# Kernel optimization log

Measured on AMD Instinct MI355X. Metric: run time of the kernel, lower is better.

## Reference

```python
import jax, jax.numpy as jnp
import numpy as np

B = 8192          # num_agents
IN_LEN = 20       # obs_len
PRED_LEN = 30     # output_len
H = 128           # h_dim
E = 64            # embedding_dim
D = 2             # data_dim
F_IN = IN_LEN * D # 40, ln1/spatial_embedding input features
LN_EPS = 1e-5


def setup_inputs() -> dict:
    key = jax.random.key(0)
    ks = jax.random.split(key, 8)
    def rn(i, shape, scale):
        return (jax.random.normal(ks[i], shape, jnp.float32) * scale).astype(jnp.float32)
    return dict(
        traj_abs=rn(0, (IN_LEN, B, D), 1.0),
        traj_rel=rn(1, (IN_LEN, B, D), 1.0),
        h0=rn(2, (1, B, H), 0.1),
        c0=rn(3, (1, B, H), 0.1),
        ln1_w=jnp.ones((F_IN,), jnp.float32),
        ln1_b=jnp.zeros((F_IN,), jnp.float32),
        emb_W=rn(4, (E, F_IN), 0.1),
        emb_b=jnp.zeros((E,), jnp.float32),
        W_ih=rn(5, (4 * H, E), 0.05),
        W_hh=rn(6, (4 * H, H), 0.05),
        b_ih=jnp.zeros((4 * H,), jnp.float32),
        b_hh=jnp.zeros((4 * H,), jnp.float32),
        ln2_w=jnp.ones((H,), jnp.float32),
        ln2_b=jnp.zeros((H,), jnp.float32),
        pos_W=rn(7, (D, H), 0.1),
        pos_b=jnp.zeros((D,), jnp.float32),
    )


def _layernorm(x, w, b):
    m = jnp.mean(x, axis=-1, keepdims=True)
    v = jnp.var(x, axis=-1, keepdims=True)
    return (x - m) * jax.lax.rsqrt(v + LN_EPS) * w + b


def reference(traj_abs, traj_rel, h0, c0, ln1_w, ln1_b, emb_W, emb_b,
              W_ih, W_hh, b_ih, b_hh, ln2_w, ln2_b, pos_W, pos_b):
    b = traj_rel.shape[1]
    h, c = h0[0], c0[0]  # num_layers=1 -> squeeze layer dim

    def step(carry, _):
        h, c, rel = carry
        # ln1 + spatial embedding + leaky_relu on raw C-order reshape (b, 40)
        x = _layernorm(rel.reshape(b, -1), ln1_w, ln1_b)
        x = jax.nn.leaky_relu(x @ emb_W.T + emb_b, negative_slope=0.01)
        # single LSTM step, torch gate order i, f, g, o
        gates = x @ W_ih.T + b_ih + h @ W_hh.T + b_hh  # (b, 4H)
        i, f, g, o = jnp.split(gates, 4, axis=-1)
        c_new = jax.nn.sigmoid(f) * c + jax.nn.sigmoid(i) * jnp.tanh(g)
        h_new = jax.nn.sigmoid(o) * jnp.tanh(c_new)
        # ln2 + hidden2pos
        rel_pos = _layernorm(h_new, ln2_w, ln2_b) @ pos_W.T + pos_b  # (b, 2)
        # roll window and write new rel position into last slot
        rel_new = jnp.concatenate([rel[1:], rel_pos[None]], axis=0)
        return (h_new, c_new, rel_new), rel_pos

    _, preds = jax.lax.scan(step, (h, c, traj_rel), None, length=PRED_LEN)
    return preds  # (pred_len, b, 2)
```

## Files before the change

### kernel.cpp

```cpp
#include <hip/hip_runtime.h>
#include <hip/hip_bf16.h>
#include <stdint.h>

#define K1 1.4426950408889634f
#define K2 2.8853900817779268f

typedef float f4 __attribute__((ext_vector_type(4)));
typedef float f2 __attribute__((ext_vector_type(2)));
typedef short s8v __attribute__((ext_vector_type(8)));
typedef unsigned int u32;
typedef unsigned short u16;

#define WS_WCAT  0
#define WS_WG    196608
#define WS_TE    204800
#define WS_SE    205056
#define WS_PWLN  205312
#define WS_SPW   206336
#define WS_PBE   206344
#define WS_BC    206352
#define WS_FLAGS 208400

#define C_WIN 0
#define C_RDY 1
#define C_RED 2
#define C_SWP 3
#define C_STT 4
#define C_PRD 5
#define C_FLG 6

__device__ __forceinline__ u16 f2bf(float x) {
    u32 u = __builtin_bit_cast(u32, x);
    u32 r = (u + 0x7FFFu + ((u >> 16) & 1u)) >> 16;
    return (u16)r;
}
__device__ __forceinline__ float bf2f(u16 h) {
    u32 u = ((u32)h) << 16;
    return __builtin_bit_cast(float, u);
}

__device__ __forceinline__ void waitge(u32* c, u32 v) {
    while (__hip_atomic_load(c, __ATOMIC_ACQUIRE, __HIP_MEMORY_SCOPE_WORKGROUP) < v) {}
}
__device__ __forceinline__ void waitge_s(u32* c, u32 v) {
    if (__hip_atomic_load(c, __ATOMIC_ACQUIRE, __HIP_MEMORY_SCOPE_WORKGROUP) >= v) return;
    do {
        __builtin_amdgcn_s_sleep(1);
    } while (__hip_atomic_load(c, __ATOMIC_ACQUIRE, __HIP_MEMORY_SCOPE_WORKGROUP) < v);
}
__device__ __forceinline__ void arrive(u32* c) {
    if ((threadIdx.x & 63) == 0)
        __hip_atomic_fetch_add(c, 1u, __ATOMIC_RELEASE, __HIP_MEMORY_SCOPE_WORKGROUP);
}

__global__ void prep_kernel(const float* __restrict__ ln1w, const float* __restrict__ ln1b,
                            const float* __restrict__ embW, const float* __restrict__ embB,
                            const float* __restrict__ Wih, const float* __restrict__ Whh,
                            const float* __restrict__ bih, const float* __restrict__ bhh,
                            const float* __restrict__ ln2w, const float* __restrict__ ln2b,
                            const float* __restrict__ posW, const float* __restrict__ posB,
                            char* __restrict__ ws) {
    const int tid = threadIdx.x;
    const int bid = blockIdx.x;
    u16* wcat = (u16*)(ws + WS_WCAT);

    if (bid > 0) {
        int base = (bid - 1) * 3072;
#pragma unroll 4
        for (int i = 0; i < 12; ++i) {
            int idx = base + i * 256 + tid;
            int np = idx / 192, k = idx % 192;
            int w = np >> 7, r = np & 127, nt = r >> 4, c = r & 15;
            int g = nt >> 1, jt = nt & 1;
            int n0 = (g << 7) | (w << 5) | (jt << 4) | c;
            float v = (k < 64) ? Wih[n0 * 64 + k] : Whh[n0 * 128 + (k - 64)];
            wcat[idx] = f2bf(v);
        }
        return;
    }

    u16* wg   = (u16*)(ws + WS_WG);
    float* te = (float*)(ws + WS_TE);
    float* se = (float*)(ws + WS_SE);
    float* pwln = (float*)(ws + WS_PWLN);
    float* spw  = (float*)(ws + WS_SPW);
    float* pbe  = (float*)(ws + WS_PBE);
    float* bc   = (float*)(ws + WS_BC);
    int* flags  = (int*)(ws + WS_FLAGS);
    __shared__ float pp[2][4];

    for (int idx = tid; idx < 64 * 64; idx += 256) {
        int e = idx >> 6, k = idx & 63;
        float v = (k < 40) ? embW[e * 40 + k] * ln1w[k] : 0.0f;
        wg[idx] = f2bf(v);
    }
    if (tid < 64) {
        int e = tid;
        float t = embB[e], s = 0.f;
        for (int k = 0; k < 40; ++k) {
            t += embW[e * 40 + k] * ln1b[k];
            s += bf2f(f2bf(embW[e * 40 + k] * ln1w[k]));
        }
        te[e] = t; se[e] = s;
    }
    if (tid >= 64 && tid < 192) {
        int j = tid - 64;
        float a0 = posW[j] * ln2w[j],      a1 = posW[128 + j] * ln2w[j];
        float b0 = posW[j] * ln2b[j],      b1 = posW[128 + j] * ln2b[j];
        pwln[j] = a0; pwln[128 + j] = a1;
#pragma unroll
        for (int m = 1; m < 64; m <<= 1) {
            a0 += __shfl_xor(a0, m, 64); a1 += __shfl_xor(a1, m, 64);
            b0 += __shfl_xor(b0, m, 64); b1 += __shfl_xor(b1, m, 64);
        }
        if ((tid & 63) == 0) {
            int wv = (tid >> 6) - 1;
            pp[wv][0] = a0; pp[wv][1] = a1; pp[wv][2] = b0; pp[wv][3] = b1;
        }
    }
    for (int idx = tid; idx < 512; idx += 256) {
        int w = idx >> 7, r = idx & 127, nt = r >> 4, c = r & 15;
        int g = nt >> 1, jt = nt & 1;
        int n0 = (g << 7) | (w << 5) | (jt << 4) | c;
        bc[idx] = bih[n0] + bhh[n0];
    }
    flags[tid] = 0;
    __syncthreads();
    if (tid == 0) {
        spw[0] = pp[0][0] + pp[1][0];
        spw[1] = pp[0][1] + pp[1][1];
        pbe[0] = posB[0] + pp[0][2] + pp[1][2];
        pbe[1] = posB[1] + pp[0][3] + pp[1][3];
    }
}

__global__ __launch_bounds__(512, 1)
void lstm_kernel(const float* __restrict__ traj_rel,
                 const float* __restrict__ h0, const float* __restrict__ c0,
                 float* __restrict__ dout, char* __restrict__ ws) {
    __shared__ __align__(16) u16 s_whh[12 * 512 * 8];
    __shared__ __align__(16) u16 s_x[2 * 8 * 32 * 8];
    __shared__ __align__(16) u16 s_h[2 * 16 * 32 * 8];
    __shared__ __align__(16) u16 s_win[2 * 8 * 32 * 8];
    __shared__ __align__(16) u16 s_pwb[2048];
    __shared__ __align__(16) float s_red1[4][4][32];
    __shared__ __align__(16) float s_red2[4][32];
    __shared__ __align__(16) f2 s_wp[320];
    __shared__ float s_mr[2][32][2];
    __shared__ float s_self[2][64];
    __shared__ u32 s_sync[8];

    const int tid = threadIdx.x;
    const int bk = blockIdx.x;
    const int lane = tid & 63;

    const u16* wcat = (const u16*)(ws + WS_WCAT);
    const u16* wg = (const u16*)(ws + WS_WG);
    int* flags = (int*)(ws + WS_FLAGS);

    if (tid == 0) {
        s_sync[C_WIN] = 0; s_sync[C_RDY] = 0; s_sync[C_RED] = 0;
        s_sync[C_SWP] = 0; s_sync[C_STT] = 0; s_sync[C_PRD] = 0;
        s_sync[C_FLG] = 0;
    }
    for (int idx = tid; idx < 12 * 512; idx += 512) {
        const u16* src = wcat + (idx & 511) * 192 + 96 + (idx >> 9) * 8;
        *(s8v*)(s_whh + idx * 8) = *(const s8v*)src;
    }
    {
        const float* pwln = (const float*)(ws + WS_PWLN);
        for (int idx = tid; idx < 2048; idx += 512) {
            int w = idx >> 9, rem = idx & 511;
            int ksub = rem >> 7, rem2 = rem & 127;
            int n = rem2 >> 3, i = rem2 & 7;
            int j = 32 * w + ksub * 8 + i;
            float v = (n == 0) ? 1.0f : (n == 1) ? pwln[j] : (n == 2) ? pwln[128 + j] : 0.0f;
            s_pwb[(((w * 4 + ksub) * 16) + n) * 8 + i] = f2bf(v);
        }
    }
    if (tid < 192) {
        int pb = tid / 96, r = tid % 96;
        int ch = 5 + r / 32, a = r & 31;
        s8v z = {0, 0, 0, 0, 0, 0, 0, 0};
        *(s8v*)(s_win + ((pb * 8 + ch) * 32 + a) * 8) = z;
    }
    if (tid < 320) {
        int p = 1280 * bk + 4 * tid;
        f4 v = *(const f4*)(traj_rel + p);
        int a = tid / 10, kq = (tid % 10) * 4;
        u32 lo = (u32)f2bf(v[0]) | ((u32)f2bf(v[1]) << 16);
        u32 hh = (u32)f2bf(v[2]) | ((u32)f2bf(v[3]) << 16);
        u32* dst = (u32*)(s_win + ((kq >> 3) * 32 + a) * 8 + (kq & 7));
        dst[0] = lo; dst[1] = hh;
        s_wp[tid] = f2{v[0] + v[1] + v[2] + v[3],
                       v[0] * v[0] + v[1] * v[1] + v[2] * v[2] + v[3] * v[3]};
    }
    if (tid < 256) {
        int a = tid & 31, q = tid >> 5;
        const float* hp = h0 + (bk * 32 + a) * 128 + q * 16;
        u16 hb[16];
#pragma unroll
        for (int u = 0; u < 16; ++u) hb[u] = f2bf(hp[u]);
#pragma unroll
        for (int half = 0; half < 2; ++half) {
            s8v v;
#pragma unroll
            for (int u = 0; u < 8; ++u) v[u] = (short)hb[half * 8 + u];
            *(s8v*)(s_h + ((2 * q + half) * 32 + a) * 8) = v;
        }
    }
    __syncthreads();
    if (tid < 32) {
        float s = 0.f, s2 = 0.f;
#pragma unroll
        for (int u = 0; u < 10; ++u) {
            f2 p = s_wp[tid * 10 + u];
            s += p[0]; s2 += p[1];
        }
        float m = s * (1.0f / 40.0f);
        float var = s2 * (1.0f / 40.0f) - m * m;
        s_mr[0][tid][0] = m;
        s_mr[0][tid][1] = __builtin_amdgcn_rsqf(var + 1e-5f);
    }
    __syncthreads();

    if (tid < 256) {
        const int wvi = tid >> 6;
        const int cx = lane & 15;
        const int hi4 = (lane >> 4) * 4;

        s8v wih[8][2], whhr[8];
#pragma unroll
        for (int nt = 0; nt < 8; ++nt) {
            int rowp = 128 * wvi + 16 * nt + cx;
#pragma unroll
            for (int kc = 0; kc < 2; ++kc)
                wih[nt][kc] = *(const s8v*)(wcat + rowp * 192 + kc * 32 + (lane >> 4) * 8);
            whhr[nt] = *(const s8v*)(wcat + rowp * 192 + 64 + (lane >> 4) * 8);
        }
        s8v wgf[2];
#pragma unroll
        for (int kc = 0; kc < 2; ++kc)
            wgf[kc] = *(const s8v*)(wg + (16 * wvi + cx) * 64 + kc * 32 + (lane >> 4) * 8);

        float se_l = ((const float*)(ws + WS_SE))[16 * wvi + cx];
        float te_l = ((const float*)(ws + WS_TE))[16 * wvi + cx];
        float bias[8];
#pragma unroll
        for (int nt = 0; nt < 8; ++nt)
            bias[nt] = ((const float*)(ws + WS_BC))[128 * wvi + 16 * nt + cx];
        float spw0 = ((const float*)(ws + WS_SPW))[0];
        float spw1 = ((const float*)(ws + WS_SPW))[1];
        float pbe0 = ((const float*)(ws + WS_PBE))[0];
        float pbe1 = ((const float*)(ws + WS_PBE))[1];

        float creg[2][2][4];
#pragma unroll
        for (int mt = 0; mt < 2; ++mt)
#pragma unroll
            for (int jt = 0; jt < 2; ++jt)
#pragma unroll
                for (int rg = 0; rg < 4; ++rg)
                    creg[mt][jt][rg] = c0[(bk * 32 + 16 * mt + hi4 + rg) * 128 + 32 * wvi + 16 * jt + cx];

        {
            f4 accE[2];
            accE[0] = f4{0.f, 0.f, 0.f, 0.f};
            accE[1] = f4{0.f, 0.f, 0.f, 0.f};
#pragma unroll
            for (int kc = 0; kc < 2; ++kc)
#pragma unroll
                for (int mt = 0; mt < 2; ++mt) {
                    s8v a = *(const s8v*)(s_win + ((kc * 4 + (lane >> 4)) * 32 + 16 * mt + cx) * 8);
                    accE[mt] = __builtin_amdgcn_mfma_f32_16x16x32_bf16(a, wgf[kc], accE[mt], 0, 0, 0);
                }
            int e = 16 * wvi + cx;
#pragma unroll
            for (int mt = 0; mt < 2; ++mt)
#pragma unroll
                for (int rg = 0; rg < 4; ++rg) {
                    int a = 16 * mt + hi4 + rg;
                    float m = s_mr[0][a][0], r = s_mr[0][a][1];
                    float x = r * (accE[mt][rg] - m * se_l) + te_l;
                    x = fmaxf(x, 0.f) + 0.01f * fminf(x, 0.f);
                    s_x[((e >> 3) * 32 + a) * 8 + (e & 7)] = f2bf(x);
                }
            arrive(&s_sync[C_RDY]);
        }

#pragma unroll 1
        for (int t = 0; t < 30; ++t) {
            const int pc = t & 1, pn = pc ^ 1;
            waitge(&s_sync[C_RDY], (u32)(4 * (t + 1)));

#pragma unroll
            for (int jt = 0; jt < 2; ++jt) {
                f4 acc[2][4];
#pragma unroll
                for (int mt = 0; mt < 2; ++mt)
#pragma unroll
                    for (int g = 0; g < 4; ++g) {
                        float b = bias[2 * g + jt];
                        acc[mt][g] = f4{b, b, b, b};
                    }
#pragma unroll
                for (int kc = 0; kc < 6; ++kc) {
                    s8v a0, a1;
                    if (kc < 2) {
                        a0 = *(const s8v*)(s_x + ((pc * 8 + kc * 4 + (lane >> 4)) * 32 + cx) * 8);
                        a1 = *(const s8v*)(s_x + ((pc * 8 + kc * 4 + (lane >> 4)) * 32 + 16 + cx) * 8);
                    } else {
                        int ch = (kc - 2) * 4 + (lane >> 4);
                        a0 = *(const s8v*)(s_h + ((pc * 16 + ch) * 32 + cx) * 8);
                        a1 = *(const s8v*)(s_h + ((pc * 16 + ch) * 32 + 16 + cx) * 8);
                    }
#pragma unroll
                    for (int g = 0; g < 4; ++g) {
                        int nt = 2 * g + jt;
                        s8v b;
                        if (kc < 2) b = wih[nt][kc];
                        else if (kc == 2) b = whhr[nt];
                        else b = *(const s8v*)(s_whh + (((kc - 3) * 4 + (lane >> 4)) * 512 + 128 * wvi + 16 * nt + cx) * 8);
                        acc[0][g] = __builtin_amdgcn_mfma_f32_16x16x32_bf16(a0, b, acc[0][g], 0, 0, 0);
                        acc[1][g] = __builtin_amdgcn_mfma_f32_16x16x32_bf16(a1, b, acc[1][g], 0, 0, 0);
                    }
                }
                int kk = 32 * wvi + 16 * jt + cx;
                int ch = pn * 16 + (kk >> 3);
#pragma unroll
                for (int mt = 0; mt < 2; ++mt)
#pragma unroll
                    for (int rg = 0; rg < 4; ++rg) {
                        float iv = acc[mt][0][rg];
                        float fv = acc[mt][1][rg];
                        float gv = acc[mt][2][rg];
                        float ov = acc[mt][3][rg];
                        float si = __builtin_amdgcn_rcpf(1.f + __builtin_amdgcn_exp2f(-K1 * iv));
                        float sf = __builtin_amdgcn_rcpf(1.f + __builtin_amdgcn_exp2f(-K1 * fv));
                        float so = __builtin_amdgcn_rcpf(1.f + __builtin_amdgcn_exp2f(-K1 * ov));
                        float tg = 1.f - 2.f * __builtin_amdgcn_rcpf(1.f + __builtin_amdgcn_exp2f(K2 * gv));
                        float cn = sf * creg[mt][jt][rg] + si * tg;
                        creg[mt][jt][rg] = cn;
                        float tc = 1.f - 2.f * __builtin_amdgcn_rcpf(1.f + __builtin_amdgcn_exp2f(K2 * cn));
                        float hn = so * tc;
                        int a = 16 * mt + hi4 + rg;
                        s_h[(ch * 32 + a) * 8 + (cx & 7)] = f2bf(hn);
                    }
            }

            {
                f4 d1[2], d2[2];
                d1[0] = f4{0.f, 0.f, 0.f, 0.f}; d1[1] = f4{0.f, 0.f, 0.f, 0.f};
                d2[0] = f4{0.f, 0.f, 0.f, 0.f}; d2[1] = f4{0.f, 0.f, 0.f, 0.f};
                s8v bfrag = *(const s8v*)(s_pwb + ((wvi * 4 + (lane >> 4)) * 16 + cx) * 8);
#pragma unroll
                for (int mt = 0; mt < 2; ++mt) {
                    s8v hf = *(const s8v*)(s_h + ((pn * 16 + 4 * wvi + (lane >> 4)) * 32 + 16 * mt + cx) * 8);
                    d1[mt] = __builtin_amdgcn_mfma_f32_16x16x32_bf16(hf, bfrag, d1[mt], 0, 0, 0);
                    d2[mt] = __builtin_amdgcn_mfma_f32_16x16x32_bf16(hf, hf, d2[mt], 0, 0, 0);
                }
#pragma unroll
                for (int mt = 0; mt < 2; ++mt) {
                    if (cx < 3) {
#pragma unroll
                        for (int rg = 0; rg < 4; ++rg)
                            s_red1[wvi][cx][mt * 16 + hi4 + rg] = d1[mt][rg];
                    }
                    if ((lane >> 4) == (cx >> 2))
                        s_red2[wvi][mt * 16 + cx] = d2[mt][cx & 3];
                }
            }
            arrive(&s_sync[C_RED]);

            if (wvi == 0) {
                waitge(&s_sync[C_RED], (u32)(4 * (t + 1)));
                int a = lane & 31, d = lane >> 5;
                float S0 = 0.f, S1 = 0.f, P = 0.f;
#pragma unroll
                for (int w = 0; w < 4; ++w) {
                    S0 += s_red1[w][0][a];
                    P  += s_red1[w][1 + d][a];
                    S1 += s_red2[w][a];
                }
                float m = S0 * (1.f / 128.f);
                float var = S1 * (1.f / 128.f) - m * m;
                float r = __builtin_amdgcn_rsqf(var + 1e-5f);
                float sp = (d == 0) ? spw0 : spw1;
                float pb = (d == 0) ? pbe0 : pbe1;
                float val = r * (P - m * sp) + pb;
                s_self[t & 1][2 * a + d] = val;
                if (tid == 0)
                    __hip_atomic_store(&s_sync[C_PRD], (u32)(t + 1), __ATOMIC_RELEASE, __HIP_MEMORY_SCOPE_WORKGROUP);
            }

            if (t < 29) {
                waitge(&s_sync[C_WIN], (u32)(t + 1));
                waitge(&s_sync[C_STT], (u32)(t + 1));
                f4 accE[2];
                accE[0] = f4{0.f, 0.f, 0.f, 0.f};
                accE[1] = f4{0.f, 0.f, 0.f, 0.f};
#pragma unroll
                for (int kc = 0; kc < 2; ++kc)
#pragma unroll
                    for (int mt = 0; mt < 2; ++mt) {
                        s8v a = *(const s8v*)(s_win + ((pn * 8 + kc * 4 + (lane >> 4)) * 32 + 16 * mt + cx) * 8);
                        accE[mt] = __builtin_amdgcn_mfma_f32_16x16x32_bf16(a, wgf[kc], accE[mt], 0, 0, 0);
                    }
                int e = 16 * wvi + cx;
#pragma unroll
                for (int mt = 0; mt < 2; ++mt)
#pragma unroll
                    for (int rg = 0; rg < 4; ++rg) {
                        int a = 16 * mt + hi4 + rg;
                        float m = s_mr[pn][a][0], r = s_mr[pn][a][1];
                        float x = r * (accE[mt][rg] - m * se_l) + te_l;
                        x = fmaxf(x, 0.f) + 0.01f * fminf(x, 0.f);
                        s_x[((pn * 8 + (e >> 3)) * 32 + a) * 8 + (e & 7)] = f2bf(x);
                    }
            }
            arrive(&s_sync[C_RDY]);
        }
    } else {
        const int gt = tid - 256;

        auto stage_one = [&](int ci, int s, int pb) {
            int p = 16384 * s + 1280 * bk + 4 * ci;
            float v0, v1, v2, v3;
            if (p < 327680) {
                f4 vv = *(const f4*)(traj_rel + p);
                v0 = vv[0]; v1 = vv[1]; v2 = vv[2]; v3 = vv[3];
            } else if (bk == 255 && ci >= 304) {
                waitge_s(&s_sync[C_PRD], (u32)s);
                int o = 4 * ci - 1216;
                const float* sf = &s_self[(s - 1) & 1][0];
                v0 = sf[o]; v1 = sf[o + 1]; v2 = sf[o + 2]; v3 = sf[o + 3];
            } else {
                waitge_s(&s_sync[C_FLG], (u32)s);
                int q = p - 327680;
                f4 vv = *(const f4*)(dout + q);
                v0 = vv[0]; v1 = vv[1]; v2 = vv[2]; v3 = vv[3];
            }
            int a = ci / 10, kq = (ci % 10) * 4;
            u32 lo = (u32)f2bf(v0) | ((u32)f2bf(v1) << 16);
            u32 hh = (u32)f2bf(v2) | ((u32)f2bf(v3) << 16);
            u32* dst = (u32*)(s_win + ((pb * 8 + (kq >> 3)) * 32 + a) * 8 + (kq & 7));
            dst[0] = lo; dst[1] = hh;
            s_wp[ci] = f2{v0 + v1 + v2 + v3, v0 * v0 + v1 * v1 + v2 * v2 + v3 * v3};
        };

#pragma unroll 1
        for (int u = 0; u < 29; ++u) {
            const int pb = (u + 1) & 1;
            waitge_s(&s_sync[C_STT], (u32)u);
            waitge_s(&s_sync[C_RDY], (u32)(4 * u));

            if (gt < 64) {
                int W0n = 16384 * (u + 1) + 1280 * bk;
                int Wend = W0n + 1280;
                if (Wend > 327680) {
                    int q0 = (W0n > 327680) ? (W0n - 327680) : 0;
                    int g = (q0 >> 6) + gt;
                    int gend = (Wend - 327681) >> 6;
                    if (g <= gend) {
                        int s = g >> 8, P = g & 255;
                        if (!(bk == 255 && P == 255)) {
                            while (__hip_atomic_load(&flags[P], __ATOMIC_RELAXED, __HIP_MEMORY_SCOPE_AGENT) <= s)
                                __builtin_amdgcn_s_sleep(2);
                        }
                    }
                }
                if (gt == 0)
                    __hip_atomic_store(&s_sync[C_FLG], (u32)(u + 1), __ATOMIC_RELEASE, __HIP_MEMORY_SCOPE_WORKGROUP);
            }

            stage_one(gt, u + 1, pb);
            if (gt < 64) stage_one(gt + 256, u + 1, pb);

            arrive(&s_sync[C_SWP]);

            if ((gt >> 6) == 1) {
                waitge_s(&s_sync[C_PRD], (u32)(u + 1));
                float val = s_self[u & 1][gt & 63];
                __hip_atomic_store(dout + u * 16384 + bk * 64 + (gt & 63), val,
                                   __ATOMIC_RELAXED, __HIP_MEMORY_SCOPE_AGENT);
                asm volatile("s_waitcnt vmcnt(0)" ::: "memory");
                if (gt == 64)
                    __hip_atomic_store(&flags[bk], u + 1, __ATOMIC_RELAXED, __HIP_MEMORY_SCOPE_AGENT);
            }

            if (gt < 64) {
                waitge_s(&s_sync[C_SWP], (u32)(4 * (u + 1)));
                if (gt == 0)
                    __hip_atomic_store(&s_sync[C_WIN], (u32)(u + 1), __ATOMIC_RELEASE, __HIP_MEMORY_SCOPE_WORKGROUP);
                if (gt < 32) {
                    float s = 0.f, s2 = 0.f;
#pragma unroll
                    for (int u2 = 0; u2 < 10; ++u2) {
                        f2 pp = s_wp[gt * 10 + u2];
                        s += pp[0]; s2 += pp[1];
                    }
                    float m = s * (1.0f / 40.0f);
                    float var = s2 * (1.0f / 40.0f) - m * m;
                    s_mr[pb][gt][0] = m;
                    s_mr[pb][gt][1] = __builtin_amdgcn_rsqf(var + 1e-5f);
                }
                if (gt == 0)
                    __hip_atomic_store(&s_sync[C_STT], (u32)(u + 1), __ATOMIC_RELEASE, __HIP_MEMORY_SCOPE_WORKGROUP);
            }
        }

        if ((gt >> 6) == 1) {
            waitge_s(&s_sync[C_PRD], 30u);
            float val = s_self[1][gt & 63];
            __hip_atomic_store(dout + 29 * 16384 + bk * 64 + (gt & 63), val,
                               __ATOMIC_RELAXED, __HIP_MEMORY_SCOPE_AGENT);
        }
    }
}

extern "C" void kernel_launch(void* const* d_in, const int* in_sizes, int n_in,
                              void* d_out, int out_size, void* d_ws, size_t ws_size,
                              hipStream_t stream) {
    (void)in_sizes; (void)n_in; (void)out_size; (void)ws_size;
    const float* traj_rel = (const float*)d_in[1];
    const float* h0 = (const float*)d_in[2];
    const float* c0 = (const float*)d_in[3];
    const float* ln1w = (const float*)d_in[4];
    const float* ln1b = (const float*)d_in[5];
    const float* embW = (const float*)d_in[6];
    const float* embB = (const float*)d_in[7];
    const float* Wih = (const float*)d_in[8];
    const float* Whh = (const float*)d_in[9];
    const float* bih = (const float*)d_in[10];
    const float* bhh = (const float*)d_in[11];
    const float* ln2w = (const float*)d_in[12];
    const float* ln2b = (const float*)d_in[13];
    const float* posW = (const float*)d_in[14];
    const float* posB = (const float*)d_in[15];
    char* ws = (char*)d_ws;

    hipLaunchKernelGGL(prep_kernel, dim3(33), dim3(256), 0, stream,
                       ln1w, ln1b, embW, embB, Wih, Whh, bih, bhh, ln2w, ln2b, posW, posB, ws);
    hipLaunchKernelGGL(lstm_kernel, dim3(256), dim3(512), 0, stream,
                       traj_rel, h0, c0, (float*)d_out, ws);
}
```

Measured before the change: 140.8 us.

## Split LSTM gate work across eight compute waves per block instead of four

Raises the block size from 512 to 768 threads so the recurrent gate MFMA work is spread over 8 waves, each handling one jt half of its wave-group's columns. Work after the gates is divided by jt: jt=0 waves do the LN2/projection reduction and jt=1 waves compute the next embedding. A new per-group barrier counter makes jt=0 wait for both halves' h writes. This aims to shorten the serial per-step critical path, at the cost of more synchronisation, more register pressure per SIMD and extra arrive counts.

```diff
diff --git a/kernel.cpp b/kernel.cpp
--- a/kernel.cpp
+++ b/kernel.cpp
@@ -28,6 +28,7 @@
 #define C_STT 4
 #define C_PRD 5
 #define C_FLG 6
+#define C_PW0 7
 
 __device__ __forceinline__ u16 f2bf(float x) {
     u32 u = __builtin_bit_cast(u32, x);
@@ -134,7 +135,7 @@
     }
 }
 
-__global__ __launch_bounds__(512, 1)
+__global__ __launch_bounds__(768, 1)
 void lstm_kernel(const float* __restrict__ traj_rel,
                  const float* __restrict__ h0, const float* __restrict__ c0,
                  float* __restrict__ dout, char* __restrict__ ws) {
@@ -148,7 +149,7 @@
     __shared__ __align__(16) f2 s_wp[320];
     __shared__ float s_mr[2][32][2];
     __shared__ float s_self[2][64];
-    __shared__ u32 s_sync[8];
+    __shared__ u32 s_sync[12];
 
     const int tid = threadIdx.x;
     const int bk = blockIdx.x;
@@ -158,18 +159,14 @@
     const u16* wg = (const u16*)(ws + WS_WG);
     int* flags = (int*)(ws + WS_FLAGS);
 
-    if (tid == 0) {
-        s_sync[C_WIN] = 0; s_sync[C_RDY] = 0; s_sync[C_RED] = 0;
-        s_sync[C_SWP] = 0; s_sync[C_STT] = 0; s_sync[C_PRD] = 0;
-        s_sync[C_FLG] = 0;
-    }
-    for (int idx = tid; idx < 12 * 512; idx += 512) {
+    if (tid < 12) s_sync[tid] = 0;
+    for (int idx = tid; idx < 12 * 512; idx += 768) {
         const u16* src = wcat + (idx & 511) * 192 + 96 + (idx >> 9) * 8;
         *(s8v*)(s_whh + idx * 8) = *(const s8v*)src;
     }
     {
         const float* pwln = (const float*)(ws + WS_PWLN);
-        for (int idx = tid; idx < 2048; idx += 512) {
+        for (int idx = tid; idx < 2048; idx += 768) {
             int w = idx >> 9, rem = idx & 511;
             int ksub = rem >> 7, rem2 = rem & 127;
             int n = rem2 >> 3, i = rem2 & 7;
@@ -224,19 +221,21 @@
     }
     __syncthreads();
 
-    if (tid < 256) {
-        const int wvi = tid >> 6;
+    if (tid < 512) {
+        const int w = tid >> 6;
+        const int wvi = w >> 1;
+        const int jt = w & 1;
         const int cx = lane & 15;
         const int hi4 = (lane >> 4) * 4;
 
-        s8v wih[8][2], whhr[8];
-#pragma unroll
-        for (int nt = 0; nt < 8; ++nt) {
-            int rowp = 128 * wvi + 16 * nt + cx;
+        s8v wih[4][2], whhr[4];
+#pragma unroll
+        for (int g = 0; g < 4; ++g) {
+            int rowp = 128 * wvi + 16 * (2 * g + jt) + cx;
 #pragma unroll
             for (int kc = 0; kc < 2; ++kc)
-                wih[nt][kc] = *(const s8v*)(wcat + rowp * 192 + kc * 32 + (lane >> 4) * 8);
-            whhr[nt] = *(const s8v*)(wcat + rowp * 192 + 64 + (lane >> 4) * 8);
+                wih[g][kc] = *(const s8v*)(wcat + rowp * 192 + kc * 32 + (lane >> 4) * 8);
+            whhr[g] = *(const s8v*)(wcat + rowp * 192 + 64 + (lane >> 4) * 8);
         }
         s8v wgf[2];
 #pragma unroll
@@ -245,25 +244,23 @@
 
         float se_l = ((const float*)(ws + WS_SE))[16 * wvi + cx];
         float te_l = ((const float*)(ws + WS_TE))[16 * wvi + cx];
-        float bias[8];
-#pragma unroll
-        for (int nt = 0; nt < 8; ++nt)
-            bias[nt] = ((const float*)(ws + WS_BC))[128 * wvi + 16 * nt + cx];
+        float bias[4];
+#pragma unroll
+        for (int g = 0; g < 4; ++g)
+            bias[g] = ((const float*)(ws + WS_BC))[128 * wvi + 16 * (2 * g + jt) + cx];
         float spw0 = ((const float*)(ws + WS_SPW))[0];
         float spw1 = ((const float*)(ws + WS_SPW))[1];
         float pbe0 = ((const float*)(ws + WS_PBE))[0];
         float pbe1 = ((const float*)(ws + WS_PBE))[1];
 
-        float creg[2][2][4];
+        float creg[2][4];
 #pragma unroll
         for (int mt = 0; mt < 2; ++mt)
 #pragma unroll
-            for (int jt = 0; jt < 2; ++jt)
-#pragma unroll
-                for (int rg = 0; rg < 4; ++rg)
-                    creg[mt][jt][rg] = c0[(bk * 32 + 16 * mt + hi4 + rg) * 128 + 32 * wvi + 16 * jt + cx];
-
-        {
+            for (int rg = 0; rg < 4; ++rg)
+                creg[mt][rg] = c0[(bk * 32 + 16 * mt + hi4 + rg) * 128 + 32 * wvi + 16 * jt + cx];
+
+        if (jt == 1) {
             f4 accE[2];
             accE[0] = f4{0.f, 0.f, 0.f, 0.f};
             accE[1] = f4{0.f, 0.f, 0.f, 0.f};
@@ -285,46 +282,43 @@
                     x = fmaxf(x, 0.f) + 0.01f * fminf(x, 0.f);
                     s_x[((e >> 3) * 32 + a) * 8 + (e & 7)] = f2bf(x);
                 }
-            arrive(&s_sync[C_RDY]);
-        }
+        }
+        arrive(&s_sync[C_RDY]);
 
 #pragma unroll 1
         for (int t = 0; t < 30; ++t) {
             const int pc = t & 1, pn = pc ^ 1;
-            waitge(&s_sync[C_RDY], (u32)(4 * (t + 1)));
-
-#pragma unroll
-            for (int jt = 0; jt < 2; ++jt) {
-                f4 acc[2][4];
-#pragma unroll
-                for (int mt = 0; mt < 2; ++mt)
-#pragma unroll
-                    for (int g = 0; g < 4; ++g) {
-                        float b = bias[2 * g + jt];
-                        acc[mt][g] = f4{b, b, b, b};
-                    }
-#pragma unroll
-                for (int kc = 0; kc < 6; ++kc) {
-                    s8v a0, a1;
-                    if (kc < 2) {
-                        a0 = *(const s8v*)(s_x + ((pc * 8 + kc * 4 + (lane >> 4)) * 32 + cx) * 8);
-                        a1 = *(const s8v*)(s_x + ((pc * 8 + kc * 4 + (lane >> 4)) * 32 + 16 + cx) * 8);
-                    } else {
-                        int ch = (kc - 2) * 4 + (lane >> 4);
-                        a0 = *(const s8v*)(s_h + ((pc * 16 + ch) * 32 + cx) * 8);
-                        a1 = *(const s8v*)(s_h + ((pc * 16 + ch) * 32 + 16 + cx) * 8);
-                    }
-#pragma unroll
-                    for (int g = 0; g < 4; ++g) {
-                        int nt = 2 * g + jt;
-                        s8v b;
-                        if (kc < 2) b = wih[nt][kc];
-                        else if (kc == 2) b = whhr[nt];
-                        else b = *(const s8v*)(s_whh + (((kc - 3) * 4 + (lane >> 4)) * 512 + 128 * wvi + 16 * nt + cx) * 8);
-                        acc[0][g] = __builtin_amdgcn_mfma_f32_16x16x32_bf16(a0, b, acc[0][g], 0, 0, 0);
-                        acc[1][g] = __builtin_amdgcn_mfma_f32_16x16x32_bf16(a1, b, acc[1][g], 0, 0, 0);
-                    }
-                }
+            waitge(&s_sync[C_RDY], (u32)(8 * (t + 1)));
+
+            f4 acc[2][4];
+#pragma unroll
+            for (int mt = 0; mt < 2; ++mt)
+#pragma unroll
+                for (int g = 0; g < 4; ++g)
+                    acc[mt][g] = f4{bias[g], bias[g], bias[g], bias[g]};
+#pragma unroll
+            for (int kc = 0; kc < 6; ++kc) {
+                s8v a0, a1;
+                if (kc < 2) {
+                    a0 = *(const s8v*)(s_x + ((pc * 8 + kc * 4 + (lane >> 4)) * 32 + cx) * 8);
+                    a1 = *(const s8v*)(s_x + ((pc * 8 + kc * 4 + (lane >> 4)) * 32 + 16 + cx) * 8);
+                } else {
+                    int ch = (kc - 2) * 4 + (lane >> 4);
+                    a0 = *(const s8v*)(s_h + ((pc * 16 + ch) * 32 + cx) * 8);
+                    a1 = *(const s8v*)(s_h + ((pc * 16 + ch) * 32 + 16 + cx) * 8);
+                }
+#pragma unroll
+                for (int g = 0; g < 4; ++g) {
+                    s8v b;
+                    if (kc < 2) b = wih[g][kc];
+                    else if (kc == 2) b = whhr[g];
+                    else b = *(const s8v*)(s_whh + (((kc - 3) * 4 + (lane >> 4)) * 512 + 128 * wvi + 16 * (2 * g + jt) + cx) * 8);
+                    acc[0][g] = __builtin_amdgcn_mfma_f32_16x16x32_bf16(a0, b, acc[0][g], 0, 0, 0);
+                    acc[1][g] = __builtin_amdgcn_mfma_f32_16x16x32_bf16(a1, b, acc[1][g], 0, 0, 0);
+                }
+            }
+
+            {
                 int kk = 32 * wvi + 16 * jt + cx;
                 int ch = pn * 16 + (kk >> 3);
 #pragma unroll
@@ -339,16 +333,18 @@
                         float sf = __builtin_amdgcn_rcpf(1.f + __builtin_amdgcn_exp2f(-K1 * fv));
                         float so = __builtin_amdgcn_rcpf(1.f + __builtin_amdgcn_exp2f(-K1 * ov));
                         float tg = 1.f - 2.f * __builtin_amdgcn_rcpf(1.f + __builtin_amdgcn_exp2f(K2 * gv));
-                        float cn = sf * creg[mt][jt][rg] + si * tg;
-                        creg[mt][jt][rg] = cn;
+                        float cn = sf * creg[mt][rg] + si * tg;
+                        creg[mt][rg] = cn;
                         float tc = 1.f - 2.f * __builtin_amdgcn_rcpf(1.f + __builtin_amdgcn_exp2f(K2 * cn));
                         float hn = so * tc;
                         int a = 16 * mt + hi4 + rg;
                         s_h[(ch * 32 + a) * 8 + (cx & 7)] = f2bf(hn);
                     }
             }
-
-            {
+            arrive(&s_sync[C_PW0 + wvi]);
+
+            if (jt == 0) {
+                waitge(&s_sync[C_PW0 + wvi], (u32)(2 * (t + 1)));
                 f4 d1[2], d2[2];
                 d1[0] = f4{0.f, 0.f, 0.f, 0.f}; d1[1] = f4{0.f, 0.f, 0.f, 0.f};
                 d2[0] = f4{0.f, 0.f, 0.f, 0.f}; d2[1] = f4{0.f, 0.f, 0.f, 0.f};
@@ -369,59 +365,59 @@
                     if ((lane >> 4) == (cx >> 2))
                         s_red2[wvi][mt * 16 + cx] = d2[mt][cx & 3];
                 }
-            }
-            arrive(&s_sync[C_RED]);
-
-            if (wvi == 0) {
-                waitge(&s_sync[C_RED], (u32)(4 * (t + 1)));
-                int a = lane & 31, d = lane >> 5;
-                float S0 = 0.f, S1 = 0.f, P = 0.f;
-#pragma unroll
-                for (int w = 0; w < 4; ++w) {
-                    S0 += s_red1[w][0][a];
-                    P  += s_red1[w][1 + d][a];
-                    S1 += s_red2[w][a];
-                }
-                float m = S0 * (1.f / 128.f);
-                float var = S1 * (1.f / 128.f) - m * m;
-                float r = __builtin_amdgcn_rsqf(var + 1e-5f);
-                float sp = (d == 0) ? spw0 : spw1;
-                float pb = (d == 0) ? pbe0 : pbe1;
-                float val = r * (P - m * sp) + pb;
-                s_self[t & 1][2 * a + d] = val;
-                if (tid == 0)
-                    __hip_atomic_store(&s_sync[C_PRD], (u32)(t + 1), __ATOMIC_RELEASE, __HIP_MEMORY_SCOPE_WORKGROUP);
-            }
-
-            if (t < 29) {
-                waitge(&s_sync[C_WIN], (u32)(t + 1));
-                waitge(&s_sync[C_STT], (u32)(t + 1));
-                f4 accE[2];
-                accE[0] = f4{0.f, 0.f, 0.f, 0.f};
-                accE[1] = f4{0.f, 0.f, 0.f, 0.f};
-#pragma unroll
-                for (int kc = 0; kc < 2; ++kc)
-#pragma unroll
-                    for (int mt = 0; mt < 2; ++mt) {
-                        s8v a = *(const s8v*)(s_win + ((pn * 8 + kc * 4 + (lane >> 4)) * 32 + 16 * mt + cx) * 8);
-                        accE[mt] = __builtin_amdgcn_mfma_f32_16x16x32_bf16(a, wgf[kc], accE[mt], 0, 0, 0);
+                arrive(&s_sync[C_RED]);
+
+                if (w == 0) {
+                    waitge(&s_sync[C_RED], (u32)(4 * (t + 1)));
+                    int a = lane & 31, d = lane >> 5;
+                    float S0 = 0.f, S1 = 0.f, P = 0.f;
+#pragma unroll
+                    for (int v = 0; v < 4; ++v) {
+                        S0 += s_red1[v][0][a];
+                        P  += s_red1[v][1 + d][a];
+                        S1 += s_red2[v][a];
                     }
-                int e = 16 * wvi + cx;
-#pragma unroll
-                for (int mt = 0; mt < 2; ++mt)
-#pragma unroll
-                    for (int rg = 0; rg < 4; ++rg) {
-                        int a = 16 * mt + hi4 + rg;
-                        float m = s_mr[pn][a][0], r = s_mr[pn][a][1];
-                        float x = r * (accE[mt][rg] - m * se_l) + te_l;
-                        x = fmaxf(x, 0.f) + 0.01f * fminf(x, 0.f);
-                        s_x[((pn * 8 + (e >> 3)) * 32 + a) * 8 + (e & 7)] = f2bf(x);
-                    }
+                    float m = S0 * (1.f / 128.f);
+                    float var = S1 * (1.f / 128.f) - m * m;
+                    float r = __builtin_amdgcn_rsqf(var + 1e-5f);
+                    float sp = (d == 0) ? spw0 : spw1;
+                    float pb = (d == 0) ? pbe0 : pbe1;
+                    float val = r * (P - m * sp) + pb;
+                    s_self[t & 1][2 * a + d] = val;
+                    if (tid == 0)
+                        __hip_atomic_store(&s_sync[C_PRD], (u32)(t + 1), __ATOMIC_RELEASE, __HIP_MEMORY_SCOPE_WORKGROUP);
+                }
+            } else {
+                if (t < 29) {
+                    waitge(&s_sync[C_WIN], (u32)(t + 1));
+                    waitge(&s_sync[C_STT], (u32)(t + 1));
+                    f4 accE[2];
+                    accE[0] = f4{0.f, 0.f, 0.f, 0.f};
+                    accE[1] = f4{0.f, 0.f, 0.f, 0.f};
+#pragma unroll
+                    for (int kc = 0; kc < 2; ++kc)
+#pragma unroll
+                        for (int mt = 0; mt < 2; ++mt) {
+                            s8v a = *(const s8v*)(s_win + ((pn * 8 + kc * 4 + (lane >> 4)) * 32 + 16 * mt + cx) * 8);
+                            accE[mt] = __builtin_amdgcn_mfma_f32_16x16x32_bf16(a, wgf[kc], accE[mt], 0, 0, 0);
+                        }
+                    int e = 16 * wvi + cx;
+#pragma unroll
+                    for (int mt = 0; mt < 2; ++mt)
+#pragma unroll
+                        for (int rg = 0; rg < 4; ++rg) {
+                            int a = 16 * mt + hi4 + rg;
+                            float m = s_mr[pn][a][0], r = s_mr[pn][a][1];
+                            float x = r * (accE[mt][rg] - m * se_l) + te_l;
+                            x = fmaxf(x, 0.f) + 0.01f * fminf(x, 0.f);
+                            s_x[((pn * 8 + (e >> 3)) * 32 + a) * 8 + (e & 7)] = f2bf(x);
+                        }
+                }
             }
             arrive(&s_sync[C_RDY]);
         }
     } else {
-        const int gt = tid - 256;
+        const int gt = tid - 512;
 
         auto stage_one = [&](int ci, int s, int pb) {
             int p = 16384 * s + 1280 * bk + 4 * ci;
@@ -452,7 +448,7 @@
         for (int u = 0; u < 29; ++u) {
             const int pb = (u + 1) & 1;
             waitge_s(&s_sync[C_STT], (u32)u);
-            waitge_s(&s_sync[C_RDY], (u32)(4 * u));
+            waitge_s(&s_sync[C_RDY], (u32)(8 * u));
 
             if (gt < 64) {
                 int W0n = 16384 * (u + 1) + 1280 * bk;
@@ -541,6 +537,6 @@
 
     hipLaunchKernelGGL(prep_kernel, dim3(33), dim3(256), 0, stream,
                        ln1w, ln1b, embW, embB, Wih, Whh, bih, bhh, ln2w, ln2b, posW, posB, ws);
-    hipLaunchKernelGGL(lstm_kernel, dim3(256), dim3(512), 0, stream,
+    hipLaunchKernelGGL(lstm_kernel, dim3(256), dim3(768), 0, stream,
                        traj_rel, h0, c0, (float*)d_out, ws);
 }
```

Result: slower. 149.7 us (+6.3%).
